# Performance work log

Measured on AMD Instinct MI355X. Metric: run time of the kernel, lower is better.

The kernel has to match this reference:

```python
import jax, jax.numpy as jnp
import numpy as np

N, E = 50000, 1600000
IN_CH, TOTAL_OUT, HEADS, NUM_LAYERS = 128, 64, 4, 3
C = TOTAL_OUT // HEADS  # out channels per head = 16
NEG_SLOPE = 0.2


def setup_inputs() -> dict:
    key = jax.random.key(0)
    ks = jax.random.split(key, 20)
    inp = {
        'x': jax.random.normal(ks[0], (N, IN_CH), dtype=jnp.float32),
        'edge_index': jax.random.randint(ks[1], (2, E), 0, N, dtype=jnp.int64),
    }
    ki = 2
    for i in range(NUM_LAYERS):
        fan_in = IN_CH if i == 0 else TOTAL_OUT
        s = 1.0 / np.sqrt(fan_in)
        inp[f'W{i}'] = jax.random.uniform(ks[ki], (fan_in, HEADS * C), jnp.float32, -s, s); ki += 1
        inp[f'att_src{i}'] = jax.random.uniform(ks[ki], (HEADS, C), jnp.float32, -s, s); ki += 1
        inp[f'att_dst{i}'] = jax.random.uniform(ks[ki], (HEADS, C), jnp.float32, -s, s); ki += 1
        inp[f'b{i}'] = jnp.zeros((HEADS * C,), dtype=jnp.float32)
    return inp


def gat_layer(x, src, dst, W, att_src, att_dst, b):
    n = x.shape[0]
    h = (x @ W).reshape(n, HEADS, C)                      # [N,H,C]
    a_s = (h * att_src).sum(-1)                            # [N,H]
    a_d = (h * att_dst).sum(-1)                            # [N,H]
    e = jax.nn.leaky_relu(a_s[src] + a_d[dst], NEG_SLOPE)  # [E',H]
    # segment softmax over incoming edges of each dst node
    m = jax.ops.segment_max(e, dst, num_segments=n)        # [N,H]
    ex = jnp.exp(e - m[dst])
    denom = jax.ops.segment_sum(ex, dst, num_segments=n)   # [N,H]
    alpha = ex / (denom[dst] + 1e-16)                      # [E',H]
    out = jax.ops.segment_sum(h[src] * alpha[:, :, None], dst, num_segments=n)  # [N,H,C]
    return out.reshape(n, HEADS * C) + b


def reference(x, edge_index, W0, att_src0, att_dst0, b0,
              W1, att_src1, att_dst1, b1,
              W2, att_src2, att_dst2, b2) -> jnp.ndarray:
    n = x.shape[0]
    loop = jnp.arange(n, dtype=edge_index.dtype)
    src = jnp.concatenate([edge_index[0], loop])  # add_self_loops=True (PyG default)
    dst = jnp.concatenate([edge_index[1], loop])
    params = [(W0, att_src0, att_dst0, b0), (W1, att_src1, att_dst1, b1), (W2, att_src2, att_dst2, b2)]
    h = x
    for i, (W, a_s, a_d, b) in enumerate(params):
        h = gat_layer(h, src, dst, W, a_s, a_d, b)
        if i < NUM_LAYERS - 1:
            h = jax.nn.relu(h)
    return h
```

## Files before the change

kernel.cpp:

```cpp
#include <hip/hip_runtime.h>
#include <hip/hip_fp16.h>
#include <math.h>

#define NN 50000
#define EE 1600000
#define HEADS 4
#define OUTC 64
#define NEG_SLOPE 0.2f

#define BM 64
#define BK 64

#define NB 196
#define RECTOT (EE + NN)
#define PCHUNK 4096
#define PGRID ((RECTOT + PCHUNK - 1) / PCHUNK)
#define BINCAP 9500
#define GEMM_BLKS 782
#define GEMM_A 391
#define GEMM_B 391


__device__ __forceinline__ void partition_body(
        int* bh, int* bbase, int blk,
        const int* __restrict__ src, const int* __restrict__ dst,
        int* __restrict__ fill1, unsigned* __restrict__ bucket) {
    int t = (int)threadIdx.x;
    if (t < NB) bh[t] = 0;
    __syncthreads();
    int base = blk * PCHUNK;
    int dv[16], sv[16], lr[16];
    #pragma unroll
    for (int j = 0; j < 16; ++j) {
        int i = base + j * 256 + t;
        bool valid = i < RECTOT;
        int d = -1, s = 0;
        if (valid) {
            if (i < EE) { d = dst[i]; s = src[i]; }
            else        { d = i - EE; s = d; }
        }
        dv[j] = d; sv[j] = s;
        lr[j] = valid ? atomicAdd(&bh[d >> 8], 1) : 0;
    }
    __syncthreads();
    if (t < NB && bh[t]) bbase[t] = atomicAdd(&fill1[t], bh[t]);
    __syncthreads();
    #pragma unroll
    for (int j = 0; j < 16; ++j) {
        if (dv[j] >= 0) {
            int bin = dv[j] >> 8;
            int pos = bbase[bin] + lr[j];
            if (pos < BINCAP)
                bucket[(size_t)bin * BINCAP + pos] =
                    ((unsigned)(dv[j] & 255) << 16) | (unsigned)sv[j];
        }
    }
}

__device__ __forceinline__ void seg_sort_body(
        unsigned char* smem, int b,
        const unsigned* __restrict__ bucket, const int* __restrict__ binStart,
        int* __restrict__ rowptr, unsigned short* __restrict__ col) {
    unsigned* stage = (unsigned*)smem;
    int* h2   = (int*)(smem + 38016);
    int* b2   = h2 + 256;
    int* c2   = b2 + 256;
    int* wsum = c2 + 256;
    int t = (int)threadIdx.x, lane = t & 63, w = t >> 6;
    int segbase = binStart[b], segend = binStart[b + 1];
    int len = segend - segbase;
    const unsigned* __restrict__ bin = bucket + (size_t)b * BINCAP;
    h2[t] = 0; c2[t] = 0;
    __syncthreads();
    for (int i = t; i < len; i += 256) {
        unsigned r = bin[i];
        stage[i] = r;
        atomicAdd(&h2[(r >> 16) & 255], 1);
    }
    __syncthreads();
    int v = h2[t], s = v;
    #pragma unroll
    for (int off = 1; off < 64; off <<= 1) {
        int u = __shfl_up(s, off);
        if (lane >= off) s += u;
    }
    if (lane == 63) wsum[w] = s;
    __syncthreads();
    int add = 0;
    for (int i = 0; i < w; ++i) add += wsum[i];
    int excl = add + s - v;
    b2[t] = excl;
    int d = (b << 8) + t;
    if (d < NN) rowptr[d] = segbase + excl;
    __syncthreads();
    for (int i = t; i < len; i += 256) {
        unsigned r = stage[i];
        int low = (r >> 16) & 255;
        int pos = b2[low] + atomicAdd(&c2[low], 1);
        col[segbase + pos] = (unsigned short)(r & 0xFFFFu);
    }
}

__device__ __forceinline__ void gemm_body(
        float (*Xt)[BM + 4], float (*Ws)[OUTC + 4], int gblk,
        const float* __restrict__ x, const float* __restrict__ W,
        const float* __restrict__ att_src, const float* __restrict__ att_dst,
        __half* __restrict__ h16,
        float* __restrict__ a_s, float* __restrict__ a_d,
        int n, int K) {
    int tid = (int)threadIdx.x;
    int tx = tid & 15, ty = tid >> 4;
    int row0 = gblk * BM;

    float acc[4][4] = {};

    for (int k0 = 0; k0 < K; k0 += BK) {
        {
            int rb = tid >> 4;
            int kb = tid & 15;
            float4 v0, v1, v2, v3;
            {
                int r0 = row0 + 4 * rb;
                int ra = r0 + 0; if (ra >= n) ra = n - 1;
                int rbx = r0 + 1; if (rbx >= n) rbx = n - 1;
                int rc = r0 + 2; if (rc >= n) rc = n - 1;
                int rd = r0 + 3; if (rd >= n) rd = n - 1;
                const float* xb = x + (size_t)k0 + 4 * kb;
                v0 = *(const float4*)(xb + (size_t)ra * K);
                v1 = *(const float4*)(xb + (size_t)rbx * K);
                v2 = *(const float4*)(xb + (size_t)rc * K);
                v3 = *(const float4*)(xb + (size_t)rd * K);
            }
            *(float4*)&Xt[4 * kb + 0][4 * rb] = make_float4(v0.x, v1.x, v2.x, v3.x);
            *(float4*)&Xt[4 * kb + 1][4 * rb] = make_float4(v0.y, v1.y, v2.y, v3.y);
            *(float4*)&Xt[4 * kb + 2][4 * rb] = make_float4(v0.z, v1.z, v2.z, v3.z);
            *(float4*)&Xt[4 * kb + 3][4 * rb] = make_float4(v0.w, v1.w, v2.w, v3.w);
        }
        {
            int k = tid >> 2;
            int c = (tid & 3) * 16;
            const float4* wp = (const float4*)(W + (size_t)(k0 + k) * OUTC + c);
            float4 v0 = wp[0], v1 = wp[1], v2 = wp[2], v3 = wp[3];
            *(float4*)&Ws[k][c]      = v0;
            *(float4*)&Ws[k][c + 4]  = v1;
            *(float4*)&Ws[k][c + 8]  = v2;
            *(float4*)&Ws[k][c + 12] = v3;
        }
        __syncthreads();
        #pragma unroll 8
        for (int k = 0; k < BK; ++k) {
            float4 xv = *(const float4*)&Xt[k][ty * 4];
            float4 wv = *(const float4*)&Ws[k][tx * 4];
            acc[0][0] = fmaf(xv.x, wv.x, acc[0][0]); acc[0][1] = fmaf(xv.x, wv.y, acc[0][1]);
            acc[0][2] = fmaf(xv.x, wv.z, acc[0][2]); acc[0][3] = fmaf(xv.x, wv.w, acc[0][3]);
            acc[1][0] = fmaf(xv.y, wv.x, acc[1][0]); acc[1][1] = fmaf(xv.y, wv.y, acc[1][1]);
            acc[1][2] = fmaf(xv.y, wv.z, acc[1][2]); acc[1][3] = fmaf(xv.y, wv.w, acc[1][3]);
            acc[2][0] = fmaf(xv.z, wv.x, acc[2][0]); acc[2][1] = fmaf(xv.z, wv.y, acc[2][1]);
            acc[2][2] = fmaf(xv.z, wv.z, acc[2][2]); acc[2][3] = fmaf(xv.z, wv.w, acc[2][3]);
            acc[3][0] = fmaf(xv.w, wv.x, acc[3][0]); acc[3][1] = fmaf(xv.w, wv.y, acc[3][1]);
            acc[3][2] = fmaf(xv.w, wv.z, acc[3][2]); acc[3][3] = fmaf(xv.w, wv.w, acc[3][3]);
        }
        __syncthreads();
    }

    float as0 = att_src[tx * 4 + 0], as1 = att_src[tx * 4 + 1];
    float as2 = att_src[tx * 4 + 2], as3 = att_src[tx * 4 + 3];
    float ad0 = att_dst[tx * 4 + 0], ad1 = att_dst[tx * 4 + 1];
    float ad2 = att_dst[tx * 4 + 2], ad3 = att_dst[tx * 4 + 3];
    int head = tx >> 2;
    #pragma unroll
    for (int i = 0; i < 4; ++i) {
        int row = row0 + ty * 4 + i;
        bool ok = row < n;
        if (ok) {
            union { __half2 h2[2]; uint2 u; } pk;
            pk.h2[0] = __floats2half2_rn(acc[i][0], acc[i][1]);
            pk.h2[1] = __floats2half2_rn(acc[i][2], acc[i][3]);
            *(uint2*)(h16 + (size_t)row * OUTC + tx * 4) = pk.u;
        }
        float ps = acc[i][0] * as0 + acc[i][1] * as1 + acc[i][2] * as2 + acc[i][3] * as3;
        float pd = acc[i][0] * ad0 + acc[i][1] * ad1 + acc[i][2] * ad2 + acc[i][3] * ad3;
        ps += __shfl_xor(ps, 1); ps += __shfl_xor(ps, 2);
        pd += __shfl_xor(pd, 1); pd += __shfl_xor(pd, 2);
        if (ok && (tx & 3) == 0) {
            a_s[row * HEADS + head] = ps;
            a_d[row * HEADS + head] = pd;
        }
    }
}


__global__ __launch_bounds__(256) void fused_part_gemm(
        const int* __restrict__ src, const int* __restrict__ dst,
        int* __restrict__ fill1, unsigned* __restrict__ bucket,
        const float* __restrict__ x, const float* __restrict__ W,
        const float* __restrict__ att_src, const float* __restrict__ att_dst,
        __half* __restrict__ h16, float* __restrict__ a_s, float* __restrict__ a_d,
        int n, int K) {
    __shared__ float Xt[BK][BM + 4];
    __shared__ float Ws[BK][OUTC + 4];
    __shared__ int bh[NB], bbase[NB];
    int b = (int)blockIdx.x;
    if (b < PGRID) partition_body(bh, bbase, b, src, dst, fill1, bucket);
    else           gemm_body(Xt, Ws, b - PGRID, x, W, att_src, att_dst, h16, a_s, a_d, n, K);
}

__global__ void scan_hi_kernel(const int* __restrict__ fill1, int* __restrict__ binStart,
                               int* __restrict__ rowptr) {
    int t = threadIdx.x, lane = t & 63, w = t >> 6;
    __shared__ int wsum[4];
    int v = (t < NB) ? fill1[t] : 0;
    int s = v;
    #pragma unroll
    for (int off = 1; off < 64; off <<= 1) {
        int u = __shfl_up(s, off);
        if (lane >= off) s += u;
    }
    if (lane == 63) wsum[w] = s;
    __syncthreads();
    int add = 0;
    for (int i = 0; i < w; ++i) add += wsum[i];
    int excl = add + s - v;
    if (t <= NB) binStart[t] = excl;
    if (t == 0) rowptr[NN] = RECTOT;
}

__global__ __launch_bounds__(256) void fused_sort_gemm(
        const unsigned* __restrict__ bucket, const int* __restrict__ binStart,
        int* __restrict__ rowptr, unsigned short* __restrict__ col,
        const float* __restrict__ x, const float* __restrict__ W,
        const float* __restrict__ att_src, const float* __restrict__ att_dst,
        __half* __restrict__ h16, float* __restrict__ a_s, float* __restrict__ a_d,
        int n, int K) {
    __shared__ __align__(16) unsigned char smem[41216];
    int b = (int)blockIdx.x;
    if (b < NB) {
        seg_sort_body(smem, b, bucket, binStart, rowptr, col);
    } else {
        float (*Xt)[BM + 4]   = (float(*)[BM + 4])smem;
        float (*Ws)[OUTC + 4] = (float(*)[OUTC + 4])(smem + sizeof(float) * BK * (BM + 4));
        gemm_body(Xt, Ws, GEMM_A + (b - NB), x, W, att_src, att_dst, h16, a_s, a_d, n, K);
    }
}

__global__ __launch_bounds__(256) void gemm_att_kernel(
        const float* __restrict__ x, const float* __restrict__ W,
        const float* __restrict__ att_src, const float* __restrict__ att_dst,
        __half* __restrict__ h16, float* __restrict__ a_s, float* __restrict__ a_d,
        int n, int K) {
    __shared__ float Xt[BK][BM + 4];
    __shared__ float Ws[BK][OUTC + 4];
    gemm_body(Xt, Ws, (int)blockIdx.x, x, W, att_src, att_dst, h16, a_s, a_d, n, K);
}

__global__ __launch_bounds__(256) void gat_aggr16_kernel(
        const int* __restrict__ rowptr, const unsigned short* __restrict__ col,
        const __half* __restrict__ h16, const float* __restrict__ a_s,
        const float* __restrict__ a_d, const float* __restrict__ bias,
        float* __restrict__ out, int n, int do_relu) {
    int node = __builtin_amdgcn_readfirstlane(
        (int)((blockIdx.x * 256u + threadIdx.x) >> 6));
    if (node >= n) return;
    int lane = (int)(threadIdx.x & 63);
    int slot = lane >> 3;
    int cl   = lane & 7;
    int head = cl >> 1;

    int beg = rowptr[node], end = rowptr[node + 1];
    float ad_h = a_d[(node << 2) | head];
    const uint4* __restrict__ hp = (const uint4*)h16;

    float4 a0 = make_float4(0.f, 0.f, 0.f, 0.f);
    float4 a1 = make_float4(0.f, 0.f, 0.f, 0.f);
    float den = 0.f;
    int e = beg + slot;
    for (; e + 8 < end; e += 16) {
        int s0 = (int)col[e], s1 = (int)col[e + 8];
        float as0 = a_s[(s0 << 2) | head];
        float as1 = a_s[(s1 << 2) | head];
        uint4 r0 = hp[(s0 << 3) | cl];
        uint4 r1 = hp[(s1 << 3) | cl];
        float x0 = as0 + ad_h; x0 = fmaxf(x0, NEG_SLOPE * x0);
        float x1 = as1 + ad_h; x1 = fmaxf(x1, NEG_SLOPE * x1);
        float e0 = __expf(x0), e1 = __expf(x1);
        union { uint4 u; __half2 h2[4]; } p0, p1;
        p0.u = r0; p1.u = r1;
        float2 f;
        f = __half22float2(p0.h2[0]); a0.x = fmaf(e0, f.x, a0.x); a0.y = fmaf(e0, f.y, a0.y);
        f = __half22float2(p0.h2[1]); a0.z = fmaf(e0, f.x, a0.z); a0.w = fmaf(e0, f.y, a0.w);
        f = __half22float2(p0.h2[2]); a1.x = fmaf(e0, f.x, a1.x); a1.y = fmaf(e0, f.y, a1.y);
        f = __half22float2(p0.h2[3]); a1.z = fmaf(e0, f.x, a1.z); a1.w = fmaf(e0, f.y, a1.w);
        f = __half22float2(p1.h2[0]); a0.x = fmaf(e1, f.x, a0.x); a0.y = fmaf(e1, f.y, a0.y);
        f = __half22float2(p1.h2[1]); a0.z = fmaf(e1, f.x, a0.z); a0.w = fmaf(e1, f.y, a0.w);
        f = __half22float2(p1.h2[2]); a1.x = fmaf(e1, f.x, a1.x); a1.y = fmaf(e1, f.y, a1.y);
        f = __half22float2(p1.h2[3]); a1.z = fmaf(e1, f.x, a1.z); a1.w = fmaf(e1, f.y, a1.w);
        den += e0 + e1;
    }
    for (; e < end; e += 8) {
        int s0 = (int)col[e];
        float as0 = a_s[(s0 << 2) | head];
        uint4 r0 = hp[(s0 << 3) | cl];
        float x0 = as0 + ad_h; x0 = fmaxf(x0, NEG_SLOPE * x0);
        float e0 = __expf(x0);
        union { uint4 u; __half2 h2[4]; } p0;
        p0.u = r0;
        float2 f;
        f = __half22float2(p0.h2[0]); a0.x = fmaf(e0, f.x, a0.x); a0.y = fmaf(e0, f.y, a0.y);
        f = __half22float2(p0.h2[1]); a0.z = fmaf(e0, f.x, a0.z); a0.w = fmaf(e0, f.y, a0.w);
        f = __half22float2(p0.h2[2]); a1.x = fmaf(e0, f.x, a1.x); a1.y = fmaf(e0, f.y, a1.y);
        f = __half22float2(p0.h2[3]); a1.z = fmaf(e0, f.x, a1.z); a1.w = fmaf(e0, f.y, a1.w);
        den += e0;
    }
    #pragma unroll
    for (int off = 8; off <= 32; off <<= 1) {
        a0.x += __shfl_xor(a0.x, off); a0.y += __shfl_xor(a0.y, off);
        a0.z += __shfl_xor(a0.z, off); a0.w += __shfl_xor(a0.w, off);
        a1.x += __shfl_xor(a1.x, off); a1.y += __shfl_xor(a1.y, off);
        a1.z += __shfl_xor(a1.z, off); a1.w += __shfl_xor(a1.w, off);
        den  += __shfl_xor(den, off);
    }
    if (slot == 0) {
        float inv = 1.0f / (den + 1e-16f);
        float4 b0 = ((const float4*)bias)[cl * 2];
        float4 b1 = ((const float4*)bias)[cl * 2 + 1];
        float4 r0 = make_float4(fmaf(a0.x, inv, b0.x), fmaf(a0.y, inv, b0.y),
                                fmaf(a0.z, inv, b0.z), fmaf(a0.w, inv, b0.w));
        float4 r1 = make_float4(fmaf(a1.x, inv, b1.x), fmaf(a1.y, inv, b1.y),
                                fmaf(a1.z, inv, b1.z), fmaf(a1.w, inv, b1.w));
        if (do_relu) {
            r0.x = fmaxf(r0.x, 0.f); r0.y = fmaxf(r0.y, 0.f);
            r0.z = fmaxf(r0.z, 0.f); r0.w = fmaxf(r0.w, 0.f);
            r1.x = fmaxf(r1.x, 0.f); r1.y = fmaxf(r1.y, 0.f);
            r1.z = fmaxf(r1.z, 0.f); r1.w = fmaxf(r1.w, 0.f);
        }
        ((float4*)out)[(node << 4) | (cl << 1)]       = r0;
        ((float4*)out)[((node << 4) | (cl << 1)) + 1] = r1;
    }
}

extern "C" void kernel_launch(void* const* d_in, const int* in_sizes, int n_in,
                              void* d_out, int out_size, void* d_ws, size_t ws_size,
                              hipStream_t stream) {
    const float* x  = (const float*)d_in[0];
    const int*   ei = (const int*)d_in[1];
    const int*   srcv = ei;
    const int*   dstv = ei + EE;

    const float* W[3]  = { (const float*)d_in[2], (const float*)d_in[6],  (const float*)d_in[10] };
    const float* AS[3] = { (const float*)d_in[3], (const float*)d_in[7],  (const float*)d_in[11] };
    const float* AD[3] = { (const float*)d_in[4], (const float*)d_in[8],  (const float*)d_in[12] };
    const float* B[3]  = { (const float*)d_in[5], (const float*)d_in[9],  (const float*)d_in[13] };

    char* ws = (char*)d_ws;
    size_t off = 0;
    auto carve = [&](size_t bytes) -> char* {
        char* p = ws + off;
        off = (off + bytes + 255) & ~(size_t)255;
        return p;
    };
    int*            rowptr   = (int*)carve((NN + 1) * sizeof(int));
    int*            fill1    = (int*)carve(NB * sizeof(int));
    int*            binStart = (int*)carve((NB + 1) * sizeof(int));
    unsigned short* colv     = (unsigned short*)carve((size_t)RECTOT * sizeof(unsigned short));
    unsigned* bucket = (unsigned*)carve((size_t)NB * BINCAP * sizeof(unsigned));
    __half*   h16    = (__half*)carve((size_t)NN * OUTC * sizeof(__half));
    float* xbuf     = (float*)carve((size_t)NN * OUTC * sizeof(float));
    float* a_s      = (float*)carve((size_t)NN * HEADS * sizeof(float));
    float* a_d      = (float*)carve((size_t)NN * HEADS * sizeof(float));

    int grid_aggr = (NN + 3) / 4;

    hipMemsetAsync(fill1, 0, NB * sizeof(int), stream);
    fused_part_gemm<<<PGRID + GEMM_A, 256, 0, stream>>>(
        srcv, dstv, fill1, bucket,
        x, W[0], AS[0], AD[0], h16, a_s, a_d, NN, 128);
    scan_hi_kernel<<<1, 256, 0, stream>>>(fill1, binStart, rowptr);
    fused_sort_gemm<<<NB + GEMM_B, 256, 0, stream>>>(
        bucket, binStart, rowptr, colv,
        x, W[0], AS[0], AD[0], h16, a_s, a_d, NN, 128);

    gat_aggr16_kernel<<<grid_aggr, 256, 0, stream>>>(rowptr, colv, h16, a_s, a_d, B[0], xbuf, NN, 1);
    gemm_att_kernel<<<GEMM_BLKS, 256, 0, stream>>>(xbuf, W[1], AS[1], AD[1], h16, a_s, a_d, NN, 64);
    gat_aggr16_kernel<<<grid_aggr, 256, 0, stream>>>(rowptr, colv, h16, a_s, a_d, B[1], xbuf, NN, 1);
    gemm_att_kernel<<<GEMM_BLKS, 256, 0, stream>>>(xbuf, W[2], AS[2], AD[2], h16, a_s, a_d, NN, 64);
    gat_aggr16_kernel<<<grid_aggr, 256, 0, stream>>>(rowptr, colv, h16, a_s, a_d, B[2], (float*)d_out, NN, 0);
}
```

Baseline: 179.1 us.

## Recompute source attention logits from gathered features in aggregation; fold bin scan into sort

The aggregation kernel no longer reads a precomputed per-node a_s array. It recomputes each edge's source attention score as a dot product of the already-gathered fp16 feature row with att_src, then combines the two lanes of a head with a shuffle. This removes the a_s store from the GEMM kernels and one scattered 4-byte load per edge. The separate single-block scan_hi kernel is dropped: every sort block now redundantly scans the bin counts itself, which removes one launch at the cost of a little extra work and shared memory per block. The per-edge math in the aggregation loop grows (about 8 FMAs plus a shuffle per edge), and the logits now come from fp16-rounded features, which could shift results slightly.

```diff
diff --git a/kernel.cpp b/kernel.cpp
--- a/kernel.cpp
+++ b/kernel.cpp
@@ -59,19 +59,37 @@
 
 __device__ __forceinline__ void seg_sort_body(
         unsigned char* smem, int b,
-        const unsigned* __restrict__ bucket, const int* __restrict__ binStart,
+        const unsigned* __restrict__ bucket, const int* __restrict__ fill1,
         int* __restrict__ rowptr, unsigned short* __restrict__ col) {
     unsigned* stage = (unsigned*)smem;
-    int* h2   = (int*)(smem + 38016);
-    int* b2   = h2 + 256;
-    int* c2   = b2 + 256;
-    int* wsum = c2 + 256;
+    int* h2    = (int*)(smem + 38016);
+    int* b2    = (int*)(smem + 39040);
+    int* c2    = (int*)(smem + 40064);
+    int* wsum  = (int*)(smem + 41088);
+    int* sfill = (int*)(smem + 41104);
     int t = (int)threadIdx.x, lane = t & 63, w = t >> 6;
-    int segbase = binStart[b], segend = binStart[b + 1];
-    int len = segend - segbase;
+
+    {
+        int v = (t < NB) ? fill1[t] : 0;
+        int s = v;
+        #pragma unroll
+        for (int off = 1; off < 64; off <<= 1) {
+            int u = __shfl_up(s, off);
+            if (lane >= off) s += u;
+        }
+        if (lane == 63) wsum[w] = s;
+        h2[t] = 0; c2[t] = 0;
+        __syncthreads();
+        int add = 0;
+        for (int i = 0; i < w; ++i) add += wsum[i];
+        if (t <= NB) sfill[t] = add + s - v;
+        __syncthreads();
+    }
+    int segbase = sfill[b];
+    int len = sfill[b + 1] - segbase;
     const unsigned* __restrict__ bin = bucket + (size_t)b * BINCAP;
-    h2[t] = 0; c2[t] = 0;
-    __syncthreads();
+    if (b == 0 && t == 0) rowptr[NN] = RECTOT;
+
     for (int i = t; i < len; i += 256) {
         unsigned r = bin[i];
         stage[i] = r;
@@ -104,9 +122,8 @@
 __device__ __forceinline__ void gemm_body(
         float (*Xt)[BM + 4], float (*Ws)[OUTC + 4], int gblk,
         const float* __restrict__ x, const float* __restrict__ W,
-        const float* __restrict__ att_src, const float* __restrict__ att_dst,
-        __half* __restrict__ h16,
-        float* __restrict__ a_s, float* __restrict__ a_d,
+        const float* __restrict__ att_dst,
+        __half* __restrict__ h16, float* __restrict__ a_d,
         int n, int K) {
     int tid = (int)threadIdx.x;
     int tx = tid & 15, ty = tid >> 4;
@@ -163,8 +180,6 @@
         __syncthreads();
     }
 
-    float as0 = att_src[tx * 4 + 0], as1 = att_src[tx * 4 + 1];
-    float as2 = att_src[tx * 4 + 2], as3 = att_src[tx * 4 + 3];
     float ad0 = att_dst[tx * 4 + 0], ad1 = att_dst[tx * 4 + 1];
     float ad2 = att_dst[tx * 4 + 2], ad3 = att_dst[tx * 4 + 3];
     int head = tx >> 2;
@@ -178,14 +193,9 @@
             pk.h2[1] = __floats2half2_rn(acc[i][2], acc[i][3]);
             *(uint2*)(h16 + (size_t)row * OUTC + tx * 4) = pk.u;
         }
-        float ps = acc[i][0] * as0 + acc[i][1] * as1 + acc[i][2] * as2 + acc[i][3] * as3;
         float pd = acc[i][0] * ad0 + acc[i][1] * ad1 + acc[i][2] * ad2 + acc[i][3] * ad3;
-        ps += __shfl_xor(ps, 1); ps += __shfl_xor(ps, 2);
         pd += __shfl_xor(pd, 1); pd += __shfl_xor(pd, 2);
-        if (ok && (tx & 3) == 0) {
-            a_s[row * HEADS + head] = ps;
-            a_d[row * HEADS + head] = pd;
-        }
+        if (ok && (tx & 3) == 0) a_d[row * HEADS + head] = pd;
     }
 }
 
@@ -194,68 +204,48 @@
         const int* __restrict__ src, const int* __restrict__ dst,
         int* __restrict__ fill1, unsigned* __restrict__ bucket,
         const float* __restrict__ x, const float* __restrict__ W,
-        const float* __restrict__ att_src, const float* __restrict__ att_dst,
-        __half* __restrict__ h16, float* __restrict__ a_s, float* __restrict__ a_d,
+        const float* __restrict__ att_dst,
+        __half* __restrict__ h16, float* __restrict__ a_d,
         int n, int K) {
     __shared__ float Xt[BK][BM + 4];
     __shared__ float Ws[BK][OUTC + 4];
     __shared__ int bh[NB], bbase[NB];
     int b = (int)blockIdx.x;
     if (b < PGRID) partition_body(bh, bbase, b, src, dst, fill1, bucket);
-    else           gemm_body(Xt, Ws, b - PGRID, x, W, att_src, att_dst, h16, a_s, a_d, n, K);
-}
-
-__global__ void scan_hi_kernel(const int* __restrict__ fill1, int* __restrict__ binStart,
-                               int* __restrict__ rowptr) {
-    int t = threadIdx.x, lane = t & 63, w = t >> 6;
-    __shared__ int wsum[4];
-    int v = (t < NB) ? fill1[t] : 0;
-    int s = v;
-    #pragma unroll
-    for (int off = 1; off < 64; off <<= 1) {
-        int u = __shfl_up(s, off);
-        if (lane >= off) s += u;
-    }
-    if (lane == 63) wsum[w] = s;
-    __syncthreads();
-    int add = 0;
-    for (int i = 0; i < w; ++i) add += wsum[i];
-    int excl = add + s - v;
-    if (t <= NB) binStart[t] = excl;
-    if (t == 0) rowptr[NN] = RECTOT;
+    else           gemm_body(Xt, Ws, b - PGRID, x, W, att_dst, h16, a_d, n, K);
 }
 
 __global__ __launch_bounds__(256) void fused_sort_gemm(
-        const unsigned* __restrict__ bucket, const int* __restrict__ binStart,
+        const unsigned* __restrict__ bucket, const int* __restrict__ fill1,
         int* __restrict__ rowptr, unsigned short* __restrict__ col,
         const float* __restrict__ x, const float* __restrict__ W,
-        const float* __restrict__ att_src, const float* __restrict__ att_dst,
-        __half* __restrict__ h16, float* __restrict__ a_s, float* __restrict__ a_d,
+        const float* __restrict__ att_dst,
+        __half* __restrict__ h16, float* __restrict__ a_d,
         int n, int K) {
-    __shared__ __align__(16) unsigned char smem[41216];
+    __shared__ __align__(16) unsigned char smem[42496];
     int b = (int)blockIdx.x;
     if (b < NB) {
-        seg_sort_body(smem, b, bucket, binStart, rowptr, col);
+        seg_sort_body(smem, b, bucket, fill1, rowptr, col);
     } else {
         float (*Xt)[BM + 4]   = (float(*)[BM + 4])smem;
         float (*Ws)[OUTC + 4] = (float(*)[OUTC + 4])(smem + sizeof(float) * BK * (BM + 4));
-        gemm_body(Xt, Ws, GEMM_A + (b - NB), x, W, att_src, att_dst, h16, a_s, a_d, n, K);
+        gemm_body(Xt, Ws, GEMM_A + (b - NB), x, W, att_dst, h16, a_d, n, K);
     }
 }
 
 __global__ __launch_bounds__(256) void gemm_att_kernel(
         const float* __restrict__ x, const float* __restrict__ W,
-        const float* __restrict__ att_src, const float* __restrict__ att_dst,
-        __half* __restrict__ h16, float* __restrict__ a_s, float* __restrict__ a_d,
+        const float* __restrict__ att_dst,
+        __half* __restrict__ h16, float* __restrict__ a_d,
         int n, int K) {
     __shared__ float Xt[BK][BM + 4];
     __shared__ float Ws[BK][OUTC + 4];
-    gemm_body(Xt, Ws, (int)blockIdx.x, x, W, att_src, att_dst, h16, a_s, a_d, n, K);
+    gemm_body(Xt, Ws, (int)blockIdx.x, x, W, att_dst, h16, a_d, n, K);
 }
 
 __global__ __launch_bounds__(256) void gat_aggr16_kernel(
         const int* __restrict__ rowptr, const unsigned short* __restrict__ col,
-        const __half* __restrict__ h16, const float* __restrict__ a_s,
+        const __half* __restrict__ h16, const float* __restrict__ att_src,
         const float* __restrict__ a_d, const float* __restrict__ bias,
         float* __restrict__ out, int n, int do_relu) {
     int node = __builtin_amdgcn_readfirstlane(
@@ -268,6 +258,8 @@
 
     int beg = rowptr[node], end = rowptr[node + 1];
     float ad_h = a_d[(node << 2) | head];
+    float4 asA = ((const float4*)att_src)[cl * 2];
+    float4 asB = ((const float4*)att_src)[cl * 2 + 1];
     const uint4* __restrict__ hp = (const uint4*)h16;
 
     float4 a0 = make_float4(0.f, 0.f, 0.f, 0.f);
@@ -276,39 +268,49 @@
     int e = beg + slot;
     for (; e + 8 < end; e += 16) {
         int s0 = (int)col[e], s1 = (int)col[e + 8];
-        float as0 = a_s[(s0 << 2) | head];
-        float as1 = a_s[(s1 << 2) | head];
         uint4 r0 = hp[(s0 << 3) | cl];
         uint4 r1 = hp[(s1 << 3) | cl];
-        float x0 = as0 + ad_h; x0 = fmaxf(x0, NEG_SLOPE * x0);
-        float x1 = as1 + ad_h; x1 = fmaxf(x1, NEG_SLOPE * x1);
-        float e0 = __expf(x0), e1 = __expf(x1);
         union { uint4 u; __half2 h2[4]; } p0, p1;
         p0.u = r0; p1.u = r1;
-        float2 f;
-        f = __half22float2(p0.h2[0]); a0.x = fmaf(e0, f.x, a0.x); a0.y = fmaf(e0, f.y, a0.y);
-        f = __half22float2(p0.h2[1]); a0.z = fmaf(e0, f.x, a0.z); a0.w = fmaf(e0, f.y, a0.w);
-        f = __half22float2(p0.h2[2]); a1.x = fmaf(e0, f.x, a1.x); a1.y = fmaf(e0, f.y, a1.y);
-        f = __half22float2(p0.h2[3]); a1.z = fmaf(e0, f.x, a1.z); a1.w = fmaf(e0, f.y, a1.w);
-        f = __half22float2(p1.h2[0]); a0.x = fmaf(e1, f.x, a0.x); a0.y = fmaf(e1, f.y, a0.y);
-        f = __half22float2(p1.h2[1]); a0.z = fmaf(e1, f.x, a0.z); a0.w = fmaf(e1, f.y, a0.w);
-        f = __half22float2(p1.h2[2]); a1.x = fmaf(e1, f.x, a1.x); a1.y = fmaf(e1, f.y, a1.y);
-        f = __half22float2(p1.h2[3]); a1.z = fmaf(e1, f.x, a1.z); a1.w = fmaf(e1, f.y, a1.w);
+        float2 g0 = __half22float2(p0.h2[0]), g1 = __half22float2(p0.h2[1]);
+        float2 g2 = __half22float2(p0.h2[2]), g3 = __half22float2(p0.h2[3]);
+        float2 q0 = __half22float2(p1.h2[0]), q1 = __half22float2(p1.h2[1]);
+        float2 q2 = __half22float2(p1.h2[2]), q3 = __half22float2(p1.h2[3]);
+        float ps0 = fmaf(g0.x, asA.x, fmaf(g0.y, asA.y, fmaf(g1.x, asA.z, fmaf(g1.y, asA.w,
+                    fmaf(g2.x, asB.x, fmaf(g2.y, asB.y, fmaf(g3.x, asB.z, g3.y * asB.w)))))));
+        float ps1 = fmaf(q0.x, asA.x, fmaf(q0.y, asA.y, fmaf(q1.x, asA.z, fmaf(q1.y, asA.w,
+                    fmaf(q2.x, asB.x, fmaf(q2.y, asB.y, fmaf(q3.x, asB.z, q3.y * asB.w)))))));
+        ps0 += __shfl_xor(ps0, 1);
+        ps1 += __shfl_xor(ps1, 1);
+        float x0 = ps0 + ad_h; x0 = fmaxf(x0, NEG_SLOPE * x0);
+        float x1 = ps1 + ad_h; x1 = fmaxf(x1, NEG_SLOPE * x1);
+        float e0 = __expf(x0), e1 = __expf(x1);
+        a0.x = fmaf(e0, g0.x, a0.x); a0.y = fmaf(e0, g0.y, a0.y);
+        a0.z = fmaf(e0, g1.x, a0.z); a0.w = fmaf(e0, g1.y, a0.w);
+        a1.x = fmaf(e0, g2.x, a1.x); a1.y = fmaf(e0, g2.y, a1.y);
+        a1.z = fmaf(e0, g3.x, a1.z); a1.w = fmaf(e0, g3.y, a1.w);
+        a0.x = fmaf(e1, q0.x, a0.x); a0.y = fmaf(e1, q0.y, a0.y);
+        a0.z = fmaf(e1, q1.x, a0.z); a0.w = fmaf(e1, q1.y, a0.w);
+        a1.x = fmaf(e1, q2.x, a1.x); a1.y = fmaf(e1, q2.y, a1.y);
+        a1.z = fmaf(e1, q3.x, a1.z); a1.w = fmaf(e1, q3.y, a1.w);
         den += e0 + e1;
     }
     for (; e < end; e += 8) {
         int s0 = (int)col[e];
-        float as0 = a_s[(s0 << 2) | head];
         uint4 r0 = hp[(s0 << 3) | cl];
-        float x0 = as0 + ad_h; x0 = fmaxf(x0, NEG_SLOPE * x0);
-        float e0 = __expf(x0);
         union { uint4 u; __half2 h2[4]; } p0;
         p0.u = r0;
-        float2 f;
-        f = __half22float2(p0.h2[0]); a0.x = fmaf(e0, f.x, a0.x); a0.y = fmaf(e0, f.y, a0.y);
-        f = __half22float2(p0.h2[1]); a0.z = fmaf(e0, f.x, a0.z); a0.w = fmaf(e0, f.y, a0.w);
-        f = __half22float2(p0.h2[2]); a1.x = fmaf(e0, f.x, a1.x); a1.y = fmaf(e0, f.y, a1.y);
-        f = __half22float2(p0.h2[3]); a1.z = fmaf(e0, f.x, a1.z); a1.w = fmaf(e0, f.y, a1.w);
+        float2 g0 = __half22float2(p0.h2[0]), g1 = __half22float2(p0.h2[1]);
+        float2 g2 = __half22float2(p0.h2[2]), g3 = __half22float2(p0.h2[3]);
+        float ps0 = fmaf(g0.x, asA.x, fmaf(g0.y, asA.y, fmaf(g1.x, asA.z, fmaf(g1.y, asA.w,
+                    fmaf(g2.x, asB.x, fmaf(g2.y, asB.y, fmaf(g3.x, asB.z, g3.y * asB.w)))))));
+        ps0 += __shfl_xor(ps0, 1);
+        float x0 = ps0 + ad_h; x0 = fmaxf(x0, NEG_SLOPE * x0);
+        float e0 = __expf(x0);
+        a0.x = fmaf(e0, g0.x, a0.x); a0.y = fmaf(e0, g0.y, a0.y);
+        a0.z = fmaf(e0, g1.x, a0.z); a0.w = fmaf(e0, g1.y, a0.w);
+        a1.x = fmaf(e0, g2.x, a1.x); a1.y = fmaf(e0, g2.y, a1.y);
+        a1.z = fmaf(e0, g3.x, a1.z); a1.w = fmaf(e0, g3.y, a1.w);
         den += e0;
     }
     #pragma unroll
@@ -360,12 +362,10 @@
     };
     int*            rowptr   = (int*)carve((NN + 1) * sizeof(int));
     int*            fill1    = (int*)carve(NB * sizeof(int));
-    int*            binStart = (int*)carve((NB + 1) * sizeof(int));
     unsigned short* colv     = (unsigned short*)carve((size_t)RECTOT * sizeof(unsigned short));
     unsigned* bucket = (unsigned*)carve((size_t)NB * BINCAP * sizeof(unsigned));
     __half*   h16    = (__half*)carve((size_t)NN * OUTC * sizeof(__half));
     float* xbuf     = (float*)carve((size_t)NN * OUTC * sizeof(float));
-    float* a_s      = (float*)carve((size_t)NN * HEADS * sizeof(float));
     float* a_d      = (float*)carve((size_t)NN * HEADS * sizeof(float));
 
     int grid_aggr = (NN + 3) / 4;
@@ -373,15 +373,14 @@
     hipMemsetAsync(fill1, 0, NB * sizeof(int), stream);
     fused_part_gemm<<<PGRID + GEMM_A, 256, 0, stream>>>(
         srcv, dstv, fill1, bucket,
-        x, W[0], AS[0], AD[0], h16, a_s, a_d, NN, 128);
-    scan_hi_kernel<<<1, 256, 0, stream>>>(fill1, binStart, rowptr);
+        x, W[0], AD[0], h16, a_d, NN, 128);
     fused_sort_gemm<<<NB + GEMM_B, 256, 0, stream>>>(
-        bucket, binStart, rowptr, colv,
-        x, W[0], AS[0], AD[0], h16, a_s, a_d, NN, 128);
-
-    gat_aggr16_kernel<<<grid_aggr, 256, 0, stream>>>(rowptr, colv, h16, a_s, a_d, B[0], xbuf, NN, 1);
-    gemm_att_kernel<<<GEMM_BLKS, 256, 0, stream>>>(xbuf, W[1], AS[1], AD[1], h16, a_s, a_d, NN, 64);
-    gat_aggr16_kernel<<<grid_aggr, 256, 0, stream>>>(rowptr, colv, h16, a_s, a_d, B[1], xbuf, NN, 1);
-    gemm_att_kernel<<<GEMM_BLKS, 256, 0, stream>>>(xbuf, W[2], AS[2], AD[2], h16, a_s, a_d, NN, 64);
-    gat_aggr16_kernel<<<grid_aggr, 256, 0, stream>>>(rowptr, colv, h16, a_s, a_d, B[2], (float*)d_out, NN, 0);
-}
+        bucket, fill1, rowptr, colv,
+        x, W[0], AD[0], h16, a_d, NN, 128);
+
+    gat_aggr16_kernel<<<grid_aggr, 256, 0, stream>>>(rowptr, colv, h16, AS[0], a_d, B[0], xbuf, NN, 1);
+    gemm_att_kernel<<<GEMM_BLKS, 256, 0, stream>>>(xbuf, W[1], AD[1], h16, a_d, NN, 64);
+    gat_aggr16_kernel<<<grid_aggr, 256, 0, stream>>>(rowptr, colv, h16, AS[1], a_d, B[1], xbuf, NN, 1);
+    gemm_att_kernel<<<GEMM_BLKS, 256, 0, stream>>>(xbuf, W[2], AD[2], h16, a_d, NN, 64);
+    gat_aggr16_kernel<<<grid_aggr, 256, 0, stream>>>(rowptr, colv, h16, AS[2], a_d, B[2], (float*)d_out, NN, 0);
+}
```

New measurement: 177.1 us. About the same (-1.1%).
